# Optimization experiments

Measured on AMD Instinct MI355X. Metric: run time of the kernel, lower is better.

Reference implementation:

```python
import jax, jax.numpy as jnp
import numpy as np
import math

V, BS, D, L, H = 50257, 1024, 768, 12, 4
DH = D // H  # 192
B, T = 4, 1024


def setup_inputs() -> dict:
    key = jax.random.key(0)
    ks = jax.random.split(key, 18)
    s = 0.02
    inp = {
        "x": jax.random.randint(ks[0], (B, T), 0, V),
        "tok_emb": jax.random.normal(ks[1], (V, D), jnp.float32) * s,
        "pos_emb": jax.random.normal(ks[2], (BS, D), jnp.float32) * s,
        "ln1_s": jnp.ones((L, D), jnp.float32),
        "ln1_b": jnp.zeros((L, D), jnp.float32),
        "qkv_w": jax.random.normal(ks[3], (L, D, 3 * D), jnp.float32) * s,
        "qkv_b": jnp.zeros((L, 3 * D), jnp.float32),
        "ln2_s": jnp.ones((L, D), jnp.float32),
        "ln2_b": jnp.zeros((L, D), jnp.float32),
        "fc_w": jax.random.normal(ks[4], (L, D, 4 * D), jnp.float32) * s,
        "fc_b": jnp.zeros((L, 4 * D), jnp.float32),
        "proj_w": jax.random.normal(ks[5], (L, 4 * D, D), jnp.float32) * s,
        "proj_b": jnp.zeros((L, D), jnp.float32),
        "lnf_s": jnp.ones((D,), jnp.float32),
        "lnf_b": jnp.zeros((D,), jnp.float32),
        "head_w": jax.random.normal(ks[6], (D, V), jnp.float32) * s,
        "head_b": jnp.zeros((V,), jnp.float32),
    }
    return inp


def _ln(x, scale, shift):
    m = x.mean(-1, keepdims=True)
    v = jnp.mean((x - m) ** 2, axis=-1, keepdims=True)
    return (x - m) * jax.lax.rsqrt(v + 1e-5) * scale + shift


def _forward(x, tok_emb, pos_emb, ln1_s, ln1_b, qkv_w, qkv_b, ln2_s, ln2_b,
             fc_w, fc_b, proj_w, proj_b, lnf_s, lnf_b, head_w, head_b):
    Bx, Tx = x.shape
    h = tok_emb[x] + pos_emb[:Tx]  # [B,T,D]
    causal = jnp.tril(jnp.ones((Tx, Tx), bool))
    scale = 1.0 / math.sqrt(DH)

    def block(h, p):
        s1, b1, wq, bq, s2, b2, wf, bf, wp, bp = p
        # attention (no output projection, faithful to source)
        ln1 = _ln(h, s1, b1)
        qkv = ln1 @ wq + bq  # [B,T,3D]
        q, k, v = jnp.split(qkv, 3, axis=-1)
        q = q.reshape(Bx, Tx, H, DH)
        k = k.reshape(Bx, Tx, H, DH)
        v = v.reshape(Bx, Tx, H, DH)
        att = jnp.einsum('bthd,bshd->bhts', q, k) * scale
        att = jnp.where(causal, att, -jnp.inf)
        att = jax.nn.softmax(att, axis=-1)
        y = jnp.einsum('bhts,bshd->bthd', att, v).reshape(Bx, Tx, D)
        h = h + y
        # MLP (ReLU, despite attr named gelu in source)
        ln2 = _ln(h, s2, b2)
        m = jax.nn.relu(ln2 @ wf + bf) @ wp + bp
        return h + m, None

    h, _ = jax.lax.scan(block, h,
                        (ln1_s, ln1_b, qkv_w, qkv_b, ln2_s, ln2_b,
                         fc_w, fc_b, proj_w, proj_b))
    h = _ln(h, lnf_s, lnf_b)
    return h @ head_w + head_b  # [B,T,V]


def reference(x, tok_emb, pos_emb, ln1_s, ln1_b, qkv_w, qkv_b, ln2_s, ln2_b,
              fc_w, fc_b, proj_w, proj_b, lnf_s, lnf_b, head_w, head_b):
    return _forward(x, tok_emb, pos_emb, ln1_s, ln1_b, qkv_w, qkv_b,
                    ln2_s, ln2_b, fc_w, fc_b, proj_w, proj_b,
                    lnf_s, lnf_b, head_w, head_b)
```

## Files before the change

kernel.cpp:

```cpp
#include <hip/hip_runtime.h>
#include <stdint.h>

#define D_MODEL 768
#define NHEAD 4
#define DHEAD 192
#define SEQ 1024
#define NLAYER 12
#define NTOK 4096
#define NVOCAB 50257

typedef __attribute__((ext_vector_type(4))) float f32x4;
typedef __attribute__((ext_vector_type(4))) int i32x4;
typedef __attribute__((ext_vector_type(4))) unsigned short u16x4;

__device__ __forceinline__ unsigned short f2bf(float f) {
  unsigned u = __builtin_bit_cast(unsigned, f);
  u += 0x7FFFu + ((u >> 16) & 1u);
  return (unsigned short)(u >> 16);
}

#define GLDS(src, dst)                                                   \
  __builtin_amdgcn_global_load_lds(                                      \
      (const __attribute__((address_space(1))) void*)(src),              \
      (__attribute__((address_space(3))) void*)(dst), 16, 0, 0)

#define FENCE asm volatile("" ::: "memory")
#define BAR()                         \
  do {                                \
    FENCE;                            \
    __builtin_amdgcn_s_barrier();     \
    FENCE;                            \
  } while (0)

__global__ __launch_bounds__(256) void embed_kernel(
    const int* __restrict__ x, const float* __restrict__ tok,
    const float* __restrict__ pos, float* __restrict__ h) {
  int row = blockIdx.x;
  int t = row & (SEQ - 1);
  int id = x[row];
  const float* tp = tok + (long)id * D_MODEL;
  const float* pp = pos + (long)t * D_MODEL;
  float* hp = h + (long)row * D_MODEL;
  for (int j = threadIdx.x; j < D_MODEL; j += 256)
    hp[j] = tp[j] + pp[j];
}

__global__ __launch_bounds__(256) void ln_kernel(
    const float* __restrict__ h, const float* __restrict__ sc,
    const float* __restrict__ sh, unsigned short* __restrict__ out) {
  __shared__ float red[4];
  int row = blockIdx.x;
  const float* x = h + (long)row * D_MODEL;
  int tid = threadIdx.x;
  float v0 = x[tid], v1 = x[tid + 256], v2 = x[tid + 512];
  float s = v0 + v1 + v2;
  for (int o = 32; o > 0; o >>= 1) s += __shfl_xor(s, o);
  if ((tid & 63) == 0) red[tid >> 6] = s;
  __syncthreads();
  float mean = (red[0] + red[1] + red[2] + red[3]) * (1.0f / D_MODEL);
  __syncthreads();
  float d0 = v0 - mean, d1 = v1 - mean, d2 = v2 - mean;
  float q = d0 * d0 + d1 * d1 + d2 * d2;
  for (int o = 32; o > 0; o >>= 1) q += __shfl_xor(q, o);
  if ((tid & 63) == 0) red[tid >> 6] = q;
  __syncthreads();
  float var = (red[0] + red[1] + red[2] + red[3]) * (1.0f / D_MODEL);
  float r = rsqrtf(var + 1e-5f);
  unsigned short* op = out + (long)row * D_MODEL;
  op[tid]       = f2bf(d0 * r * sc[tid]       + sh[tid]);
  op[tid + 256] = f2bf(d1 * r * sc[tid + 256] + sh[tid + 256]);
  op[tid + 512] = f2bf(d2 * r * sc[tid + 512] + sh[tid + 512]);
}

__global__ __launch_bounds__(256) void wtrans3_kernel(
    const float* __restrict__ qw, const float* __restrict__ fw,
    const float* __restrict__ pw, unsigned short* __restrict__ tq,
    unsigned short* __restrict__ tf, unsigned short* __restrict__ tp) {
  __shared__ unsigned short tile[32][33];
  int bid = blockIdx.x;
  const float* src; unsigned short* dst; int K, N, nb;
  if (bid < 1728)               { src = qw; dst = tq; K = 768;  N = 2304; nb = 72; }
  else if ((bid -= 1728) < 2304){ src = fw; dst = tf; K = 768;  N = 3072; nb = 96; }
  else { bid -= 2304;             src = pw; dst = tp; K = 3072; N = 768;  nb = 24; }
  int n0 = (bid % nb) * 32, k0 = (bid / nb) * 32;
  int tx = threadIdx.x & 31, ty = threadIdx.x >> 5;
  #pragma unroll
  for (int i = 0; i < 4; ++i) {
    int k = k0 + ty + i * 8;
    tile[ty + i * 8][tx] = f2bf(src[(long)k * N + n0 + tx]);
  }
  __syncthreads();
  #pragma unroll
  for (int i = 0; i < 4; ++i) {
    int nn = n0 + ty + i * 8;
    dst[(long)nn * K + k0 + tx] = tile[tx][ty + i * 8];
  }
}

__global__ __launch_bounds__(256) void wtrans_kernel(
    const float* __restrict__ w, unsigned short* __restrict__ wt, int K, int N) {
  __shared__ unsigned short tile[32][33];
  int n0 = blockIdx.x * 32, k0 = blockIdx.y * 32;
  int tx = threadIdx.x, ty = threadIdx.y;
  int n = n0 + tx; if (n >= N) n = N - 1;
  #pragma unroll
  for (int i = 0; i < 4; ++i) {
    int k = k0 + ty + i * 8;
    tile[ty + i * 8][tx] = f2bf(w[(long)k * N + n]);
  }
  __syncthreads();
  #pragma unroll
  for (int i = 0; i < 4; ++i) {
    int nn = n0 + ty + i * 8;
    if (nn < N) wt[(long)nn * K + k0 + tx] = tile[tx][ty + i * 8];
  }
}

__global__ __launch_bounds__(256) void vt_kernel(
    const unsigned short* __restrict__ qkv, unsigned short* __restrict__ vt) {
  __shared__ unsigned short tile[32][33];
  int bh = blockIdx.z, b = bh >> 2, hh = bh & 3;
  int t0 = blockIdx.x * 32, f0 = blockIdx.y * 32;
  int tx = threadIdx.x, ty = threadIdx.y;
  const unsigned short* src = qkv + (long)b * SEQ * 2304 + 2 * D_MODEL + hh * DHEAD;
  #pragma unroll
  for (int i = 0; i < 4; ++i) {
    int t = t0 + ty + i * 8;
    tile[ty + i * 8][tx] = src[(long)t * 2304 + f0 + tx];
  }
  __syncthreads();
  unsigned short* dst = vt + (long)bh * DHEAD * SEQ;
  #pragma unroll
  for (int i = 0; i < 4; ++i) {
    int f = f0 + ty + i * 8;
    dst[(long)f * SEQ + t0 + tx] = tile[tx][ty + i * 8];
  }
}

__global__ __launch_bounds__(256) void qk_kernel(
    const unsigned short* __restrict__ qkv, float* __restrict__ S) {
  const float rscale = 0.07216878364870323f;
  int tid = threadIdx.x;
  int lane = tid & 63, wid = tid >> 6;
  int l15 = lane & 15, g = lane >> 4;
  int bid = blockIdx.x;
  int bh = bid & 15;
  int p = bid >> 4;
  int qt = (p & 1) ? (p >> 1) : (63 - (p >> 1));
  int b = bh >> 2, hh = bh & 3;
  const unsigned short* Qb = qkv + ((long)b * 1024 + qt * 16) * 2304 + hh * 192;
  const unsigned short* Kb = qkv + (long)b * 1024 * 2304 + 768 + hh * 192;
  float* Srow = S + ((long)bh * 1024 + qt * 16) * 1024;

  i32x4 qfr[6];
  #pragma unroll
  for (int kb = 0; kb < 6; ++kb)
    qfr[kb] = *(const i32x4*)(Qb + (long)l15 * 2304 + kb * 32 + g * 8);

  int nsf = qt + 1;
  for (int sf = wid; sf < nsf; sf += 4) {
    f32x4 sacc = {};
    #pragma unroll
    for (int kb = 0; kb < 6; ++kb) {
      i32x4 kf = *(const i32x4*)(Kb + (long)(sf * 16 + l15) * 2304 + kb * 32 + g * 8);
      asm("v_mfma_f32_16x16x32_bf16 %0, %1, %2, %0"
          : "+v"(sacc) : "v"(kf), "v"(qfr[kb]));
    }
    asm volatile("s_nop 7\n\ts_nop 7\n\ts_nop 7" : "+v"(sacc));
    f32x4 st;
    #pragma unroll
    for (int e = 0; e < 4; ++e) st[e] = sacc[e] * rscale;
    *(f32x4*)(Srow + (long)l15 * 1024 + sf * 16 + 4 * g) = st;
  }
}

__global__ __launch_bounds__(256) void softmax_kernel(
    const float* __restrict__ S, unsigned short* __restrict__ P) {
  __shared__ float red[4];
  long rid = blockIdx.x;
  int q = (int)(rid & (SEQ - 1));
  int tid = threadIdx.x;
  int i0 = tid * 4;
  f32x4 v;
  if (i0 <= q) {
    v = *(const f32x4*)(S + rid * SEQ + i0);
  } else {
    v = f32x4{-3.0e38f, -3.0e38f, -3.0e38f, -3.0e38f};
  }
  float m = -3.0e38f;
  #pragma unroll
  for (int j = 0; j < 4; ++j) {
    if (i0 + j > q) v[j] = -3.0e38f;
    m = fmaxf(m, v[j]);
  }
  for (int o = 32; o > 0; o >>= 1) m = fmaxf(m, __shfl_xor(m, o));
  if ((tid & 63) == 0) red[tid >> 6] = m;
  __syncthreads();
  m = fmaxf(fmaxf(red[0], red[1]), fmaxf(red[2], red[3]));
  __syncthreads();
  float e[4];
  float sum = 0.f;
  #pragma unroll
  for (int j = 0; j < 4; ++j) {
    e[j] = (i0 + j > q) ? 0.f : __expf(v[j] - m);
    sum += e[j];
  }
  for (int o = 32; o > 0; o >>= 1) sum += __shfl_xor(sum, o);
  if ((tid & 63) == 0) red[tid >> 6] = sum;
  __syncthreads();
  float inv = 1.0f / (red[0] + red[1] + red[2] + red[3]);
  if ((i0 >> 7) <= (q >> 7)) {
    u16x4 out;
    #pragma unroll
    for (int j = 0; j < 4; ++j) out[j] = f2bf(e[j] * inv);
    *(u16x4*)(P + rid * SEQ + i0) = out;
  }
}

template<int MODE>
__global__ __launch_bounds__(512, 2) void gemm256_kernel(
    const unsigned short* __restrict__ A,
    const unsigned short* __restrict__ B,
    const float* __restrict__ bias,
    void* __restrict__ Cv, int ldc,
    int M, int N, int K, int mb) {
  __shared__ __align__(16) unsigned short lds[2][2][2][128 * 64];

  int tid = threadIdx.x;
  int lane = tid & 63;
  int wid = tid >> 6;
  int wm = wid >> 2;
  int wn = wid & 3;

  int bid = blockIdx.x;
  int mpx = mb >> 3;
  int xcd = bid & 7;
  int c = bid >> 3;
  int m0 = (xcd * mpx + (c & (mpx - 1))) * 256;
  int n0 = (c / mpx) * 256;

  auto stageA = [&](int buf, int half, int kt) {
    const unsigned short* src = A + (long)(m0 + half * 128) * K + kt * 64;
    #pragma unroll
    for (int i = 0; i < 2; ++i) {
      int chunk = i * 8 + wid;
      int r = chunk * 8 + (lane >> 3);
      int cc = ((lane & 7) ^ (lane >> 3)) << 3;
      GLDS(src + (long)r * K + cc, &lds[buf][0][half][chunk * 512]);
    }
  };
  auto stageB = [&](int buf, int half, int kt) {
    #pragma unroll
    for (int i = 0; i < 2; ++i) {
      int chunk = i * 8 + wid;
      int r = chunk * 8 + (lane >> 3);
      int cc = ((lane & 7) ^ (lane >> 3)) << 3;
      int rg = n0 + half * 128 + r;
      if (rg >= N) rg = N - 1;
      GLDS(B + (long)rg * K + kt * 64 + cc, &lds[buf][1][half][chunk * 512]);
    }
  };

  auto lda_frag = [&](int buf, int f, int s) -> i32x4 {
    int r = wm * 64 + (f & 3) * 16 + (lane & 15);
    int kb = s * 64 + ((lane >> 4) << 4);
    int off = r * 128 + (kb ^ ((r & 7) << 4));
    return *(const i32x4*)((const char*)&lds[buf][0][f >> 2][0] + off);
  };
  auto ldb_frag = [&](int buf, int gg, int s) -> i32x4 {
    int r = wn * 32 + (gg & 1) * 16 + (lane & 15);
    int kb = s * 64 + ((lane >> 4) << 4);
    int off = r * 128 + (kb ^ ((r & 7) << 4));
    return *(const i32x4*)((const char*)&lds[buf][1][gg >> 1][0] + off);
  };

  f32x4 acc[8][4] = {};
  i32x4 a[4][2], b[4][2];

  int nt = K / 64;

  stageA(0, 0, 0); stageB(0, 0, 0); stageB(0, 1, 0); stageA(0, 1, 0);
  stageA(1, 0, 1); stageB(1, 0, 1); stageB(1, 1, 1);
  asm volatile("s_waitcnt vmcnt(6)" ::: "memory");
  BAR();

  for (int t = 0; t < nt; ++t) {
    int buf = t & 1, nbuf = buf ^ 1;
    #pragma unroll
    for (int fi = 0; fi < 4; ++fi) {
      a[fi][0] = lda_frag(buf, fi, 0);
      a[fi][1] = lda_frag(buf, fi, 1);
    }
    #pragma unroll
    for (int gi = 0; gi < 2; ++gi) {
      b[gi][0] = ldb_frag(buf, gi, 0);
      b[gi][1] = ldb_frag(buf, gi, 1);
    }
    if (t + 1 < nt) stageA(nbuf, 1, t + 1);
    BAR();
    __builtin_amdgcn_s_setprio(1);
    #pragma unroll
    for (int s = 0; s < 2; ++s)
      #pragma unroll
      for (int fi = 0; fi < 4; ++fi)
        #pragma unroll
        for (int gi = 0; gi < 2; ++gi)
          asm("v_mfma_f32_16x16x32_bf16 %0, %1, %2, %0"
              : "+v"(acc[fi][gi]) : "v"(b[gi][s]), "v"(a[fi][s]));
    __builtin_amdgcn_s_setprio(0);
    BAR();
    #pragma unroll
    for (int gi = 2; gi < 4; ++gi) {
      b[gi][0] = ldb_frag(buf, gi, 0);
      b[gi][1] = ldb_frag(buf, gi, 1);
    }
    if (t + 2 < nt) stageA(buf, 0, t + 2);
    BAR();
    __builtin_amdgcn_s_setprio(1);
    #pragma unroll
    for (int s = 0; s < 2; ++s)
      #pragma unroll
      for (int fi = 0; fi < 4; ++fi)
        #pragma unroll
        for (int gi = 2; gi < 4; ++gi)
          asm("v_mfma_f32_16x16x32_bf16 %0, %1, %2, %0"
              : "+v"(acc[fi][gi]) : "v"(b[gi][s]), "v"(a[fi][s]));
    __builtin_amdgcn_s_setprio(0);
    BAR();
    #pragma unroll
    for (int fi = 0; fi < 4; ++fi) {
      a[fi][0] = lda_frag(buf, 4 + fi, 0);
      a[fi][1] = lda_frag(buf, 4 + fi, 1);
    }
    if (t + 2 < nt) stageB(buf, 0, t + 2);
    BAR();
    __builtin_amdgcn_s_setprio(1);
    #pragma unroll
    for (int s = 0; s < 2; ++s)
      #pragma unroll
      for (int fi = 0; fi < 4; ++fi)
        #pragma unroll
        for (int gi = 2; gi < 4; ++gi)
          asm("v_mfma_f32_16x16x32_bf16 %0, %1, %2, %0"
              : "+v"(acc[4 + fi][gi]) : "v"(b[gi][s]), "v"(a[fi][s]));
    __builtin_amdgcn_s_setprio(0);
    BAR();
    if (t + 2 < nt) {
      stageB(buf, 1, t + 2);
      asm volatile("s_waitcnt vmcnt(6)" ::: "memory");
    } else if (t + 1 < nt) {
      asm volatile("s_waitcnt vmcnt(0)" ::: "memory");
    }
    BAR();
    __builtin_amdgcn_s_setprio(1);
    #pragma unroll
    for (int s = 0; s < 2; ++s)
      #pragma unroll
      for (int fi = 0; fi < 4; ++fi)
        #pragma unroll
        for (int gi = 0; gi < 2; ++gi)
          asm("v_mfma_f32_16x16x32_bf16 %0, %1, %2, %0"
              : "+v"(acc[4 + fi][gi]) : "v"(b[gi][s]), "v"(a[fi][s]));
    __builtin_amdgcn_s_setprio(0);
    BAR();
  }

  int cr = lane & 15;
  int cg = (lane >> 4) << 2;
  #pragma unroll
  for (int f = 0; f < 8; ++f) {
    long row = m0 + wm * 64 + (f & 3) * 16 + (f >> 2) * 128 + cr;
    #pragma unroll
    for (int gg = 0; gg < 4; ++gg) {
      int col = n0 + wn * 32 + (gg & 1) * 16 + (gg >> 1) * 128 + cg;
      f32x4 v = acc[f][gg];
      if (MODE == 0 || MODE == 1) {
        f32x4 bv = *(const f32x4*)(bias + col);
        u16x4 o;
        #pragma unroll
        for (int r = 0; r < 4; ++r) {
          float tt = v[r] + bv[r];
          if (MODE == 1) tt = fmaxf(tt, 0.f);
          o[r] = f2bf(tt);
        }
        *(u16x4*)((unsigned short*)Cv + row * (long)ldc + col) = o;
      } else {
        float* cp = (float*)Cv + row * (long)ldc + col;
        if (col + 4 <= N) {
          f32x4 bv = *(const f32x4*)(bias + col);
          f32x4 o;
          #pragma unroll
          for (int r = 0; r < 4; ++r) o[r] = v[r] + bv[r];
          *(f32x4*)cp = o;
        } else {
          #pragma unroll
          for (int r = 0; r < 4; ++r)
            if (col + r < N) cp[r] = v[r] + bias[col + r];
        }
      }
    }
  }
}

#define BM 128
#define BN 128
#define BKK 32

template<int MODE>
__global__ __launch_bounds__(256) void gemm_kernel(
    const unsigned short* __restrict__ A, int lda,
    const unsigned short* __restrict__ B, int ldb,
    const float* __restrict__ bias,
    void* __restrict__ Cv, int ldc,
    int M, int N, int K,
    int NI, long sAo, long sAi, long sBo, long sBi,
    long sCo, long sCi, float alpha, int causal, int mblocks) {
  __shared__ __align__(16) unsigned short As[2][BM * BKK];
  __shared__ __align__(16) unsigned short Bs[2][BN * BKK];
  int z = blockIdx.z;
  int zo = z / NI, zi = z - zo * NI;
  A += zo * sAo + zi * sAi;
  B += zo * sBo + zi * sBi;
  long coff = zo * sCo + zi * sCi;

  int m0, n0;
  if (mblocks > 0) {
    int bid = blockIdx.x;
    int mpx = mblocks >> 3;
    int xcd = bid & 7;
    int c = bid >> 3;
    m0 = (xcd * mpx + (c & (mpx - 1))) * BM;
    n0 = (c / mpx) * BN;
  } else {
    m0 = blockIdx.y * BM;
    n0 = blockIdx.x * BN;
  }
  if (causal == 1 && n0 > m0 + BM - 1) return;
  int kmax = (causal == 2) ? min(K, m0 + BM) : K;

  int tid = threadIdx.x;
  int lane = tid & 63;
  int wave = tid >> 6;
  int wm = (wave >> 1) * 64;
  int wn = (wave & 1) * 64;

  auto stage = [&](int buf, int k0) {
    #pragma unroll
    for (int i = 0; i < 2; ++i) {
      int c0 = i * 256 + wave * 64;
      int cc = c0 + lane;
      int row = cc >> 2;
      int ko = (cc & 3) << 3;
      GLDS(A + (long)(m0 + row) * lda + k0 + ko, As[buf] + c0 * 8);
      int rg = n0 + row; if (rg >= N) rg = N - 1;
      GLDS(B + (long)rg * ldb + k0 + ko, Bs[buf] + c0 * 8);
    }
  };

  f32x4 acc[4][4] = {};
  int nt = kmax / BKK;
  stage(0, 0);
  __syncthreads();
  int cur = 0;
  for (int t = 0; t < nt; ++t) {
    if (t + 1 < nt) stage(cur ^ 1, (t + 1) * BKK);
    int lr = lane & 15;
    int kg = (lane >> 4) << 3;
    i32x4 af[4], bf[4];
    #pragma unroll
    for (int mi = 0; mi < 4; ++mi)
      af[mi] = *(const i32x4*)(As[cur] + (wm + mi * 16 + lr) * BKK + kg);
    #pragma unroll
    for (int ni = 0; ni < 4; ++ni)
      bf[ni] = *(const i32x4*)(Bs[cur] + (wn + ni * 16 + lr) * BKK + kg);
    #pragma unroll
    for (int mi = 0; mi < 4; ++mi)
      #pragma unroll
      for (int ni = 0; ni < 4; ++ni)
        asm("v_mfma_f32_16x16x32_bf16 %0, %1, %2, %0"
            : "+v"(acc[mi][ni]) : "v"(bf[ni]), "v"(af[mi]));
    __syncthreads();
    cur ^= 1;
  }

  int cm = lane & 15;
  int cg = (lane >> 4) << 2;
  #pragma unroll
  for (int mi = 0; mi < 4; ++mi) {
    long row = m0 + wm + mi * 16 + cm;
    #pragma unroll
    for (int ni = 0; ni < 4; ++ni) {
      int col = n0 + wn + ni * 16 + cg;
      f32x4 v = acc[mi][ni];
      if (MODE == 2) {
        #pragma unroll
        for (int r = 0; r < 4; ++r) v[r] *= alpha;
        *(f32x4*)((float*)Cv + coff + row * (long)ldc + col) = v;
      } else if (MODE == 0 || MODE == 1) {
        f32x4 bv = *(const f32x4*)(bias + col);
        u16x4 o;
        #pragma unroll
        for (int r = 0; r < 4; ++r) {
          float t = v[r] + bv[r];
          if (MODE == 1) t = fmaxf(t, 0.f);
          o[r] = f2bf(t);
        }
        *(u16x4*)((unsigned short*)Cv + coff + row * (long)ldc + col) = o;
      } else {
        float* cp = (float*)Cv + coff + row * (long)ldc + col;
        if (col + 4 <= N) {
          f32x4 bv = bias ? *(const f32x4*)(bias + col)
                          : f32x4{0.f, 0.f, 0.f, 0.f};
          if (MODE == 3) {
            f32x4 old = *(f32x4*)cp;
            #pragma unroll
            for (int r = 0; r < 4; ++r) old[r] += v[r] + bv[r];
            *(f32x4*)cp = old;
          } else {
            f32x4 o;
            #pragma unroll
            for (int r = 0; r < 4; ++r) o[r] = v[r] + bv[r];
            *(f32x4*)cp = o;
          }
        } else {
          #pragma unroll
          for (int r = 0; r < 4; ++r) {
            if (col + r < N) {
              float bvr = bias ? bias[col + r] : 0.f;
              if (MODE == 3) cp[r] += v[r] + bvr;
              else           cp[r] = v[r] + bvr;
            }
          }
        }
      }
    }
  }
}

extern "C" void kernel_launch(void* const* d_in, const int* in_sizes, int n_in,
                              void* d_out, int out_size, void* d_ws, size_t ws_size,
                              hipStream_t stream) {
  const int*   x       = (const int*)  d_in[0];
  const float* tok_emb = (const float*)d_in[1];
  const float* pos_emb = (const float*)d_in[2];
  const float* ln1_s   = (const float*)d_in[3];
  const float* ln1_b   = (const float*)d_in[4];
  const float* qkv_w   = (const float*)d_in[5];
  const float* qkv_b   = (const float*)d_in[6];
  const float* ln2_s   = (const float*)d_in[7];
  const float* ln2_b   = (const float*)d_in[8];
  const float* fc_w    = (const float*)d_in[9];
  const float* fc_b    = (const float*)d_in[10];
  const float* proj_w  = (const float*)d_in[11];
  const float* proj_b  = (const float*)d_in[12];
  const float* lnf_s   = (const float*)d_in[13];
  const float* lnf_b   = (const float*)d_in[14];
  const float* head_w  = (const float*)d_in[15];
  const float* head_b  = (const float*)d_in[16];

  char* ws = (char*)d_ws;
  size_t off = 0;
  auto alloc = [&](size_t bytes) {
    char* p = ws + off;
    off += (bytes + 255) & ~(size_t)255;
    return p;
  };
  float*          h   = (float*)         alloc((size_t)NTOK * D_MODEL * 4);
  unsigned short* lnb = (unsigned short*)alloc((size_t)NTOK * D_MODEL * 2);
  unsigned short* qkv = (unsigned short*)alloc((size_t)NTOK * 2304 * 2);
  unsigned short* vt  = (unsigned short*)alloc((size_t)16 * DHEAD * SEQ * 2);
  unsigned short* mid = (unsigned short*)alloc((size_t)NTOK * 3072 * 2);
  float*          S   = (float*)         alloc((size_t)16 * SEQ * SEQ * 4);
  unsigned short* P   = (unsigned short*)alloc((size_t)16 * SEQ * SEQ * 2);
  unsigned short* wtq = (unsigned short*)alloc((size_t)2304 * 768 * 2);
  unsigned short* wtf = (unsigned short*)alloc((size_t)3072 * 768 * 2);
  unsigned short* wtp = (unsigned short*)alloc((size_t)768 * 3072 * 2);
  unsigned short* wth = (unsigned short*)alloc((size_t)50304 * 768 * 2);

  embed_kernel<<<NTOK, 256, 0, stream>>>(x, tok_emb, pos_emb, h);

  for (int l = 0; l < NLAYER; ++l) {
    wtrans3_kernel<<<6336, 256, 0, stream>>>(
        qkv_w + (long)l * 768 * 2304, fc_w + (long)l * 768 * 3072,
        proj_w + (long)l * 3072 * 768, wtq, wtf, wtp);
    ln_kernel<<<NTOK, 256, 0, stream>>>(h, ln1_s + l * 768, ln1_b + l * 768, lnb);
    gemm256_kernel<0><<<16 * 9, 512, 0, stream>>>(
        lnb, wtq, qkv_b + l * 2304, qkv, 2304, 4096, 2304, 768, 16);
    vt_kernel<<<dim3(32, 6, 16), dim3(32, 8), 0, stream>>>(qkv, vt);
    qk_kernel<<<1024, 256, 0, stream>>>(qkv, S);
    softmax_kernel<<<16384, 256, 0, stream>>>(S, P);
    gemm_kernel<3><<<dim3(2, 8, 16), 256, 0, stream>>>(
        P, 1024, vt, 1024, nullptr, h, 768,
        1024, 192, 1024, 4,
        (long)4 * 1024 * 1024, (long)1024 * 1024,
        (long)4 * 192 * 1024, (long)192 * 1024,
        (long)1024 * 768, 192, 1.0f, 2, 0);
    ln_kernel<<<NTOK, 256, 0, stream>>>(h, ln2_s + l * 768, ln2_b + l * 768, lnb);
    gemm256_kernel<1><<<16 * 12, 512, 0, stream>>>(
        lnb, wtf, fc_b + l * 3072, mid, 3072, 4096, 3072, 768, 16);
    gemm_kernel<3><<<192, 256, 0, stream>>>(
        mid, 3072, wtp, 3072, proj_b + l * 768, h, 768,
        4096, 768, 3072, 1, 0, 0, 0, 0, 0, 0, 1.0f, 0, 32);
  }

  wtrans_kernel<<<dim3(1571, 24), dim3(32, 8), 0, stream>>>(head_w, wth, 768, 50257);
  ln_kernel<<<NTOK, 256, 0, stream>>>(h, lnf_s, lnf_b, lnb);
  gemm256_kernel<4><<<16 * 197, 512, 0, stream>>>(
      lnb, wth, head_b, (float*)d_out, 50257, 4096, 50257, 768, 16);
}
```

Baseline: 3.427 ms.

## Fuse QK, softmax and PV into one attention kernel using LDS

Replaces the three-kernel attention path (QK scores written to a global fp32 S buffer, a separate softmax kernel writing bf16 P, then a batched GEMM over P and V) with one kernel per 16-query tile. It keeps the score row block and the probabilities in shared memory and accumulates P·V with MFMA directly into the residual. This removes the large global S and P round trips and two launches per layer. In exchange it uses 96KB of LDS per block, which limits occupancy, and the PV loop loads V straight from global memory without tiling, with only 16 queries per block.

```diff
diff --git a/kernel.cpp b/kernel.cpp
--- a/kernel.cpp
+++ b/kernel.cpp
@@ -137,8 +137,12 @@
   }
 }
 
-__global__ __launch_bounds__(256) void qk_kernel(
-    const unsigned short* __restrict__ qkv, float* __restrict__ S) {
+__global__ __launch_bounds__(256) void fattn2_kernel(
+    const unsigned short* __restrict__ qkv,
+    const unsigned short* __restrict__ vt,
+    float* __restrict__ h) {
+  __shared__ float slds[16][1024];
+  __shared__ unsigned short plds[16][1024];
   const float rscale = 0.07216878364870323f;
   int tid = threadIdx.x;
   int lane = tid & 63, wid = tid >> 6;
@@ -146,19 +150,23 @@
   int bid = blockIdx.x;
   int bh = bid & 15;
   int p = bid >> 4;
-  int qt = (p & 1) ? (p >> 1) : (63 - (p >> 1));
+  int qt = (p < 32) ? (63 - p) : (p - 32);
   int b = bh >> 2, hh = bh & 3;
   const unsigned short* Qb = qkv + ((long)b * 1024 + qt * 16) * 2304 + hh * 192;
   const unsigned short* Kb = qkv + (long)b * 1024 * 2304 + 768 + hh * 192;
-  float* Srow = S + ((long)bh * 1024 + qt * 16) * 1024;
+  const unsigned short* Vb = vt + (long)bh * 192 * 1024;
+  int smax = qt * 16 + 16;
+  int smax32 = (smax + 31) & ~31;
 
   i32x4 qfr[6];
   #pragma unroll
   for (int kb = 0; kb < 6; ++kb)
     qfr[kb] = *(const i32x4*)(Qb + (long)l15 * 2304 + kb * 32 + g * 8);
-
-  int nsf = qt + 1;
-  for (int sf = wid; sf < nsf; sf += 4) {
+  int nsf = smax >> 4;
+  int sfw = (nsf + 3) >> 2;
+  int sf0 = wid * sfw;
+  int sf1 = min(sf0 + sfw, nsf);
+  for (int sf = sf0; sf < sf1; ++sf) {
     f32x4 sacc = {};
     #pragma unroll
     for (int kb = 0; kb < 6; ++kb) {
@@ -170,50 +178,64 @@
     f32x4 st;
     #pragma unroll
     for (int e = 0; e < 4; ++e) st[e] = sacc[e] * rscale;
-    *(f32x4*)(Srow + (long)l15 * 1024 + sf * 16 + 4 * g) = st;
-  }
-}
-
-__global__ __launch_bounds__(256) void softmax_kernel(
-    const float* __restrict__ S, unsigned short* __restrict__ P) {
-  __shared__ float red[4];
-  long rid = blockIdx.x;
-  int q = (int)(rid & (SEQ - 1));
-  int tid = threadIdx.x;
-  int i0 = tid * 4;
-  f32x4 v;
-  if (i0 <= q) {
-    v = *(const f32x4*)(S + rid * SEQ + i0);
-  } else {
-    v = f32x4{-3.0e38f, -3.0e38f, -3.0e38f, -3.0e38f};
-  }
-  float m = -3.0e38f;
-  #pragma unroll
-  for (int j = 0; j < 4; ++j) {
-    if (i0 + j > q) v[j] = -3.0e38f;
-    m = fmaxf(m, v[j]);
-  }
-  for (int o = 32; o > 0; o >>= 1) m = fmaxf(m, __shfl_xor(m, o));
-  if ((tid & 63) == 0) red[tid >> 6] = m;
-  __syncthreads();
-  m = fmaxf(fmaxf(red[0], red[1]), fmaxf(red[2], red[3]));
-  __syncthreads();
-  float e[4];
-  float sum = 0.f;
-  #pragma unroll
-  for (int j = 0; j < 4; ++j) {
-    e[j] = (i0 + j > q) ? 0.f : __expf(v[j] - m);
-    sum += e[j];
-  }
-  for (int o = 32; o > 0; o >>= 1) sum += __shfl_xor(sum, o);
-  if ((tid & 63) == 0) red[tid >> 6] = sum;
-  __syncthreads();
-  float inv = 1.0f / (red[0] + red[1] + red[2] + red[3]);
-  if ((i0 >> 7) <= (q >> 7)) {
-    u16x4 out;
-    #pragma unroll
-    for (int j = 0; j < 4; ++j) out[j] = f2bf(e[j] * inv);
-    *(u16x4*)(P + rid * SEQ + i0) = out;
+    *(f32x4*)&slds[l15][sf * 16 + 4 * g] = st;
+  }
+  __syncthreads();
+
+  {
+    int q = tid >> 4, lane16 = tid & 15;
+    int qg = qt * 16 + q;
+    float mx = -3.0e38f;
+    for (int s = lane16 * 4; s < smax32; s += 64) {
+      f32x4 v = *(const f32x4*)&slds[q][s];
+      #pragma unroll
+      for (int e = 0; e < 4; ++e)
+        if (s + e <= qg) mx = fmaxf(mx, v[e]);
+    }
+    #pragma unroll
+    for (int o = 1; o < 16; o <<= 1) mx = fmaxf(mx, __shfl_xor(mx, o));
+    float sum = 0.f;
+    for (int s = lane16 * 4; s < smax32; s += 64) {
+      f32x4 v = *(const f32x4*)&slds[q][s];
+      #pragma unroll
+      for (int e = 0; e < 4; ++e)
+        v[e] = (s + e <= qg) ? __expf(v[e] - mx) : 0.f;
+      *(f32x4*)&slds[q][s] = v;
+      sum += v[0] + v[1] + v[2] + v[3];
+    }
+    #pragma unroll
+    for (int o = 1; o < 16; o <<= 1) sum += __shfl_xor(sum, o);
+    float inv = 1.0f / sum;
+    for (int s = lane16 * 4; s < smax32; s += 64) {
+      f32x4 v = *(const f32x4*)&slds[q][s];
+      u16x4 o;
+      #pragma unroll
+      for (int e = 0; e < 4; ++e) o[e] = f2bf(v[e] * inv);
+      *(u16x4*)&plds[q][s] = o;
+    }
+  }
+  __syncthreads();
+
+  f32x4 acc[3] = {};
+  for (int ss = 0; ss < smax32; ss += 32) {
+    i32x4 pf = *(const i32x4*)&plds[l15][ss + g * 8];
+    #pragma unroll
+    for (int nf = 0; nf < 3; ++nf) {
+      i32x4 vf = *(const i32x4*)(Vb + (long)(wid * 48 + nf * 16 + l15) * 1024 + ss + g * 8);
+      asm("v_mfma_f32_16x16x32_bf16 %0, %1, %2, %0"
+          : "+v"(acc[nf]) : "v"(vf), "v"(pf));
+    }
+  }
+  asm volatile("s_nop 7\n\ts_nop 7\n\ts_nop 7"
+               : "+v"(acc[0]), "+v"(acc[1]), "+v"(acc[2]));
+  float* hp = h + ((long)b * 1024 + qt * 16 + l15) * 768 + hh * 192 + wid * 48;
+  #pragma unroll
+  for (int nf = 0; nf < 3; ++nf) {
+    float* cp = hp + nf * 16 + 4 * g;
+    f32x4 old = *(f32x4*)cp;
+    #pragma unroll
+    for (int e = 0; e < 4; ++e) old[e] += acc[nf][e];
+    *(f32x4*)cp = old;
   }
 }
 
@@ -570,8 +592,6 @@
   unsigned short* qkv = (unsigned short*)alloc((size_t)NTOK * 2304 * 2);
   unsigned short* vt  = (unsigned short*)alloc((size_t)16 * DHEAD * SEQ * 2);
   unsigned short* mid = (unsigned short*)alloc((size_t)NTOK * 3072 * 2);
-  float*          S   = (float*)         alloc((size_t)16 * SEQ * SEQ * 4);
-  unsigned short* P   = (unsigned short*)alloc((size_t)16 * SEQ * SEQ * 2);
   unsigned short* wtq = (unsigned short*)alloc((size_t)2304 * 768 * 2);
   unsigned short* wtf = (unsigned short*)alloc((size_t)3072 * 768 * 2);
   unsigned short* wtp = (unsigned short*)alloc((size_t)768 * 3072 * 2);
@@ -587,14 +607,7 @@
     gemm256_kernel<0><<<16 * 9, 512, 0, stream>>>(
         lnb, wtq, qkv_b + l * 2304, qkv, 2304, 4096, 2304, 768, 16);
     vt_kernel<<<dim3(32, 6, 16), dim3(32, 8), 0, stream>>>(qkv, vt);
-    qk_kernel<<<1024, 256, 0, stream>>>(qkv, S);
-    softmax_kernel<<<16384, 256, 0, stream>>>(S, P);
-    gemm_kernel<3><<<dim3(2, 8, 16), 256, 0, stream>>>(
-        P, 1024, vt, 1024, nullptr, h, 768,
-        1024, 192, 1024, 4,
-        (long)4 * 1024 * 1024, (long)1024 * 1024,
-        (long)4 * 192 * 1024, (long)192 * 1024,
-        (long)1024 * 768, 192, 1.0f, 2, 0);
+    fattn2_kernel<<<1024, 256, 0, stream>>>(qkv, vt, h);
     ln_kernel<<<NTOK, 256, 0, stream>>>(h, ln2_s + l * 768, ln2_b + l * 768, lnb);
     gemm256_kernel<1><<<16 * 12, 512, 0, stream>>>(
         lnb, wtf, fc_b + l * 3072, mid, 3072, 4096, 3072, 768, 16);
```

New measurement: 3.258 ms. 4.9% less time.
